# Optimization experiments

Hardware: AMD Instinct MI355X
Metric: run time of the kernel (lower is better)

## Reference

```python
import jax, jax.numpy as jnp
import numpy as np

N_OUT = 4096
N_IN = 4096
NNZ = 1600000
BATCH = 4096


def setup_inputs() -> dict:
    key = jax.random.key(0)
    k1, k2, k3, k4, k5 = jax.random.split(key, 5)
    inputs = jax.random.normal(k1, (N_IN, BATCH), dtype=jnp.float32)
    values = jax.random.normal(k2, (NNZ,), dtype=jnp.float32)
    biases = jax.random.normal(k3, (N_OUT, 1), dtype=jnp.float32)
    rows = jax.random.randint(k4, (NNZ,), 0, N_OUT, dtype=jnp.int32)
    cols = jax.random.randint(k5, (NNZ,), 0, N_IN, dtype=jnp.int32)
    return {"inputs": inputs, "values": values, "biases": biases,
            "rows": rows, "cols": cols}


def reference(inputs, values, biases, rows, cols):
    # torch.sparse.addmm(biases, W_sparse, inputs) with W COO [N_OUT, N_IN].
    # Scatter-add COO entries into a dense weight (duplicates summed, matching
    # coalesce semantics), then one dense GEMM -- avoids an [NNZ, BATCH]
    # gather intermediate while computing identical math.
    W = jnp.zeros((N_OUT, N_IN), dtype=values.dtype).at[rows, cols].add(values)
    out = W @ inputs + biases  # [N_OUT, BATCH], bias broadcast over columns
    return jax.nn.relu(out)    # activation epilogue
```

## Files before the change

### kernel.cpp

```cpp
#include <hip/hip_runtime.h>
#include <stdint.h>

#define N_OUT_  4096
#define N_IN_   4096
#define BATCH_  4096
#define NNZ_    1600000

typedef unsigned short ushort_t;
typedef float  f32x4  __attribute__((ext_vector_type(4)));
typedef short  short8 __attribute__((ext_vector_type(8)));
typedef __bf16 bf16x8 __attribute__((ext_vector_type(8)));

__device__ inline ushort_t f32_to_bf16(float f) {
  uint32_t u = __float_as_uint(f);
  uint32_t r = u + 0x7FFFu + ((u >> 16) & 1u);
  return (ushort_t)(r >> 16);
}
__device__ inline float bf16_to_f32(ushort_t h) {
  return __uint_as_float(((uint32_t)h) << 16);
}

__device__ inline void gload_lds16(const void* g, void* l) {
  __builtin_amdgcn_global_load_lds(
      (const __attribute__((address_space(1))) void*)g,
      (__attribute__((address_space(3))) void*)l,
      16, 0, 0);
}

__device__ inline f32x4 mfma_bf16(short8 a, short8 b, f32x4 c) {
  return __builtin_amdgcn_mfma_f32_16x16x32_bf16(
      __builtin_bit_cast(bf16x8, a), __builtin_bit_cast(bf16x8, b), c, 0, 0, 0);
}

#define BARRIER() asm volatile("s_barrier" ::: "memory")
template <int N> __device__ __forceinline__ void waitvm() {
  if constexpr (N == 8)      asm volatile("s_waitcnt vmcnt(8)" ::: "memory");
  else if constexpr (N == 6) asm volatile("s_waitcnt vmcnt(6)" ::: "memory");
  else if constexpr (N == 4) asm volatile("s_waitcnt vmcnt(4)" ::: "memory");
  else                       asm volatile("s_waitcnt vmcnt(0)" ::: "memory");
}

__global__ __launch_bounds__(256) void scatter_coo_cas(
    const float* __restrict__ vals, const int* __restrict__ rows,
    const int* __restrict__ cols, uint32_t* __restrict__ W32) {
  int i = blockIdx.x * 256 + threadIdx.x;
  if (i >= NNZ_) return;
  const size_t idx = (size_t)rows[i] * N_IN_ + cols[i];
  const float v = vals[i];
  uint32_t* p = &W32[idx >> 1];
  const bool hi = (idx & 1) != 0;
  uint32_t old = *p, assumed;
  do {
    assumed = old;
    ushort_t h = hi ? (ushort_t)(assumed >> 16) : (ushort_t)(assumed & 0xFFFFu);
    ushort_t nh = f32_to_bf16(bf16_to_f32(h) + v);
    uint32_t nw = hi ? ((assumed & 0x0000FFFFu) | ((uint32_t)nh << 16))
                     : ((assumed & 0xFFFF0000u) | (uint32_t)nh);
    old = atomicCAS(p, assumed, nw);
  } while (old != assumed);
}

__global__ __launch_bounds__(256) void transpose_bf16(
    const float* __restrict__ in, ushort_t* __restrict__ out) {
  __shared__ float tile[32][33];
  const int bx = blockIdx.x * 32, by = blockIdx.y * 32;
  const int tx = threadIdx.x, ty = threadIdx.y;
#pragma unroll
  for (int i = 0; i < 32; i += 8)
    tile[ty + i][tx] = in[(size_t)(by + ty + i) * BATCH_ + bx + tx];
  __syncthreads();
#pragma unroll
  for (int i = 0; i < 32; i += 8)
    out[(size_t)(bx + ty + i) * N_IN_ + by + tx] = f32_to_bf16(tile[tx][ty + i]);
}

#define BM 256
#define BN 256
#define BK 32
#define KTILES 128
#define TILE_BYTES 32768
#define B_OFF 16384

__global__ __launch_bounds__(512, 2) void gemm_bias_relu(
    const ushort_t* __restrict__ A,
    const ushort_t* __restrict__ Bt,
    const float* __restrict__ bias,
    float* __restrict__ C) {
  __shared__ __align__(16) char smem[4 * TILE_BYTES];

  const int tid  = threadIdx.x;
  const int wid  = tid >> 6;
  const int lane = tid & 63;

  const int bid = blockIdx.x;
  const int swz = (bid & 7) * 32 + (bid >> 3);
  const int brow = (swz >> 4) * BM;
  const int bcol = (swz & 15) * BN;

  const int wr = wid >> 2;
  const int wc = wid & 3;
  const int fr = lane & 15;
  const int k0slot = lane >> 4;

  int aoff[8], boff[4];
#pragma unroll
  for (int mi = 0; mi < 8; ++mi) {
    int off = (wr * 128 + mi * 16 + fr) * 64 + k0slot * 16;
    aoff[mi] = off ^ (((off >> 7) & 3) << 4);
  }
#pragma unroll
  for (int ni = 0; ni < 4; ++ni) {
    int off = (wc * 64 + ni * 16 + fr) * 64 + k0slot * 16;
    boff[ni] = off ^ (((off >> 7) & 3) << 4);
  }

  const bool isB = wid >= 4;
  const int sw = isB ? wid - 4 : wid;
  const int swzl = lane ^ ((lane >> 3) & 3);
  const int rowInChunk = swzl >> 2;
  const int kelem = (swzl & 3) * 8;
  const ushort_t* gsrc = isB ? Bt : A;
  const size_t laneRowBase =
      (size_t)((isB ? bcol : brow) + sw * 64 + rowInChunk) * N_IN_ + kelem;
  const int ldsOpBase = isB ? B_OFF : 0;

#define STAGE(p, i, t)                                                        \
  gload_lds16(gsrc + laneRowBase + (size_t)(2 * (p) + (i)) * 16 * N_IN_ +     \
                  (size_t)(t) * BK,                                           \
              smem + ((t) & 3) * TILE_BYTES + ldsOpBase +                     \
                  (4 * sw + 2 * (p) + (i)) * 1024)

  f32x4 acc[8][4] = {};
  short8 aE[4], bE[4], aO[4], bO[4], aH[4];

#pragma unroll
  for (int t = 0; t < 3; ++t) {
    STAGE(0, 0, t); STAGE(0, 1, t); STAGE(1, 0, t); STAGE(1, 1, t);
  }
  waitvm<8>();
  BARRIER();
#pragma unroll
  for (int j = 0; j < 4; ++j) {
    aE[j] = *(const short8*)(smem + aoff[j]);
    bE[j] = *(const short8*)(smem + B_OFF + boff[j]);
  }

#define TILE(t, AL, BB, ALn, BBn, S_ON, VM, RA_ON)                            \
  do {                                                                        \
    const char* buf  = &smem[((t) & 3) * TILE_BYTES];                         \
    const char* bufn = &smem[(((t) + 1) & 3) * TILE_BYTES];                   \
                                                                      \
    _Pragma("unroll") for (int j = 0; j < 4; ++j)                             \
        aH[j] = *(const short8*)(buf + aoff[j + 4]);                          \
    if (S_ON) { STAGE(0, 0, (t) + 3); STAGE(0, 1, (t) + 3); }                 \
    VM;                                                                       \
    BARRIER();                                                                \
    if (RA_ON) {                                                              \
      _Pragma("unroll") for (int j = 0; j < 4; ++j)                           \
          ALn[j] = *(const short8*)(bufn + aoff[j]);                          \
    }                                                                         \
    __builtin_amdgcn_s_setprio(1);                                            \
    _Pragma("unroll") for (int mi = 0; mi < 4; ++mi)                          \
        _Pragma("unroll") for (int ni = 0; ni < 4; ++ni)                      \
            acc[mi][ni] = mfma_bf16(AL[mi], BB[ni], acc[mi][ni]);             \
    __builtin_amdgcn_s_setprio(0);                                            \
    BARRIER();                                                                \
                                                                      \
    if (RA_ON) {                                                              \
      _Pragma("unroll") for (int j = 0; j < 4; ++j)                           \
          BBn[j] = *(const short8*)(bufn + B_OFF + boff[j]);                  \
    }                                                                         \
    if (S_ON) { STAGE(1, 0, (t) + 3); STAGE(1, 1, (t) + 3); }                 \
    BARRIER();                                                                \
    __builtin_amdgcn_s_setprio(1);                                            \
    _Pragma("unroll") for (int mi = 0; mi < 4; ++mi)                          \
        _Pragma("unroll") for (int ni = 0; ni < 4; ++ni)                      \
            acc[mi + 4][ni] = mfma_bf16(aH[mi], BB[ni], acc[mi + 4][ni]);     \
    __builtin_amdgcn_s_setprio(0);                                            \
    BARRIER();                                                                \
  } while (0)

  for (int t = 0; t < KTILES - 4; t += 2) {
    TILE(t,     aE, bE, aO, bO, 1, waitvm<6>(), 1);
    TILE(t + 1, aO, bO, aE, bE, 1, waitvm<6>(), 1);
  }
  TILE(KTILES - 4, aE, bE, aO, bO, 1, waitvm<6>(), 1);
  TILE(KTILES - 3, aO, bO, aE, bE, 0, waitvm<4>(), 1);
  TILE(KTILES - 2, aE, bE, aO, bO, 0, waitvm<0>(), 1);
  TILE(KTILES - 1, aO, bO, aE, bE, 0, (void)0,     0);

  const int r0 = brow + wr * 128 + k0slot * 4;
  const int c0 = bcol + wc * 64 + fr;
#pragma unroll
  for (int mi = 0; mi < 8; ++mi) {
#pragma unroll
    for (int r = 0; r < 4; ++r) {
      const int row = r0 + mi * 16 + r;
      const float b = bias[row];
#pragma unroll
      for (int ni = 0; ni < 4; ++ni) {
        float v = acc[mi][ni][r] + b;
        C[(size_t)row * BATCH_ + c0 + ni * 16] = v > 0.f ? v : 0.f;
      }
    }
  }
#undef TILE
#undef STAGE
}

extern "C" void kernel_launch(void* const* d_in, const int* in_sizes, int n_in,
                              void* d_out, int out_size, void* d_ws, size_t ws_size,
                              hipStream_t stream) {
  const float* inputs = (const float*)d_in[0];
  const float* values = (const float*)d_in[1];
  const float* biases = (const float*)d_in[2];
  const int*   rows   = (const int*)d_in[3];
  const int*   cols   = (const int*)d_in[4];
  float* out = (float*)d_out;

  const size_t W_BF16_BYTES = (size_t)N_OUT_ * N_IN_ * 2;
  if (ws_size < 2 * W_BF16_BYTES) return;
  char* ws = (char*)d_ws;
  ushort_t* Wb = (ushort_t*)ws;
  ushort_t* Bt = (ushort_t*)(ws + W_BF16_BYTES);

  hipMemsetAsync(Wb, 0, W_BF16_BYTES, stream);
  scatter_coo_cas<<<(NNZ_ + 255) / 256, 256, 0, stream>>>(values, rows, cols,
                                                          (uint32_t*)Wb);
  transpose_bf16<<<dim3(BATCH_ / 32, N_IN_ / 32), dim3(32, 8), 0, stream>>>(inputs, Bt);
  gemm_bias_relu<<<dim3(256), 512, 0, stream>>>(Wb, Bt, biases, out);
}
```

Before: 217.7 us.

## Restructure GEMM main loop into two-tile pairs with one barrier per tile

Replaces the ping-pong register-prefetch pipeline, which had split half-tile MFMA phases and three barriers per K tile, with a simpler scheme. Each K tile now issues all four global-to-LDS stage loads at once, reads the full A and B fragments from LDS, then runs all 32 MFMAs. Tiles are processed in pairs behind a single vmcnt wait and barrier, with one more barrier between the two tiles. This cuts barrier and wait overhead, but gives up the overlap of next-tile LDS reads with the current tile's MFMAs, so LDS latency may be exposed.

```diff
diff --git a/kernel.cpp b/kernel.cpp
--- a/kernel.cpp
+++ b/kernel.cpp
@@ -35,7 +35,6 @@
 #define BARRIER() asm volatile("s_barrier" ::: "memory")
 template <int N> __device__ __forceinline__ void waitvm() {
   if constexpr (N == 8)      asm volatile("s_waitcnt vmcnt(8)" ::: "memory");
-  else if constexpr (N == 6) asm volatile("s_waitcnt vmcnt(6)" ::: "memory");
   else if constexpr (N == 4) asm volatile("s_waitcnt vmcnt(4)" ::: "memory");
   else                       asm volatile("s_waitcnt vmcnt(0)" ::: "memory");
 }
@@ -124,70 +123,44 @@
       (size_t)((isB ? bcol : brow) + sw * 64 + rowInChunk) * N_IN_ + kelem;
   const int ldsOpBase = isB ? B_OFF : 0;
 
-#define STAGE(p, i, t)                                                        \
-  gload_lds16(gsrc + laneRowBase + (size_t)(2 * (p) + (i)) * 16 * N_IN_ +     \
-                  (size_t)(t) * BK,                                           \
+#define STAGE(c, t)                                                           \
+  gload_lds16(gsrc + laneRowBase + (size_t)(c) * 16 * N_IN_ + (size_t)(t) * BK,\
               smem + ((t) & 3) * TILE_BYTES + ldsOpBase +                     \
-                  (4 * sw + 2 * (p) + (i)) * 1024)
+                  (4 * sw + (c)) * 1024)
+#define STAGE4(t) do { STAGE(0,(t)); STAGE(1,(t)); STAGE(2,(t)); STAGE(3,(t)); } while (0)
 
   f32x4 acc[8][4] = {};
-  short8 aE[4], bE[4], aO[4], bO[4], aH[4];
-
-#pragma unroll
-  for (int t = 0; t < 3; ++t) {
-    STAGE(0, 0, t); STAGE(0, 1, t); STAGE(1, 0, t); STAGE(1, 1, t);
-  }
-  waitvm<8>();
-  BARRIER();
-#pragma unroll
-  for (int j = 0; j < 4; ++j) {
-    aE[j] = *(const short8*)(smem + aoff[j]);
-    bE[j] = *(const short8*)(smem + B_OFF + boff[j]);
-  }
-
-#define TILE(t, AL, BB, ALn, BBn, S_ON, VM, RA_ON)                            \
+  short8 af[8], bf[4];
+
+  STAGE4(0); STAGE4(1); STAGE4(2);
+
+#define HALF(t, S_ON, ST)                                                     \
   do {                                                                        \
-    const char* buf  = &smem[((t) & 3) * TILE_BYTES];                         \
-    const char* bufn = &smem[(((t) + 1) & 3) * TILE_BYTES];                   \
-                                                                      \
-    _Pragma("unroll") for (int j = 0; j < 4; ++j)                             \
-        aH[j] = *(const short8*)(buf + aoff[j + 4]);                          \
-    if (S_ON) { STAGE(0, 0, (t) + 3); STAGE(0, 1, (t) + 3); }                 \
+    const char* buf = &smem[((t) & 3) * TILE_BYTES];                          \
+    if (S_ON) STAGE4(ST);                                                     \
+    _Pragma("unroll") for (int ni = 0; ni < 4; ++ni)                          \
+        bf[ni] = *(const short8*)(buf + B_OFF + boff[ni]);                    \
+    _Pragma("unroll") for (int mi = 0; mi < 8; ++mi)                          \
+        af[mi] = *(const short8*)(buf + aoff[mi]);                            \
+    __builtin_amdgcn_s_setprio(1);                                            \
+    _Pragma("unroll") for (int mi = 0; mi < 8; ++mi)                          \
+        _Pragma("unroll") for (int ni = 0; ni < 4; ++ni)                      \
+            acc[mi][ni] = mfma_bf16(af[mi], bf[ni], acc[mi][ni]);             \
+    __builtin_amdgcn_s_setprio(0);                                            \
+  } while (0)
+
+#define PAIR(t, S1, S2, VM)                                                   \
+  do {                                                                        \
     VM;                                                                       \
     BARRIER();                                                                \
-    if (RA_ON) {                                                              \
-      _Pragma("unroll") for (int j = 0; j < 4; ++j)                           \
-          ALn[j] = *(const short8*)(bufn + aoff[j]);                          \
-    }                                                                         \
-    __builtin_amdgcn_s_setprio(1);                                            \
-    _Pragma("unroll") for (int mi = 0; mi < 4; ++mi)                          \
-        _Pragma("unroll") for (int ni = 0; ni < 4; ++ni)                      \
-            acc[mi][ni] = mfma_bf16(AL[mi], BB[ni], acc[mi][ni]);             \
-    __builtin_amdgcn_s_setprio(0);                                            \
+    HALF((t), S1, (t) + 3);                                                   \
     BARRIER();                                                                \
-                                                                      \
-    if (RA_ON) {                                                              \
-      _Pragma("unroll") for (int j = 0; j < 4; ++j)                           \
-          BBn[j] = *(const short8*)(bufn + B_OFF + boff[j]);                  \
-    }                                                                         \
-    if (S_ON) { STAGE(1, 0, (t) + 3); STAGE(1, 1, (t) + 3); }                 \
-    BARRIER();                                                                \
-    __builtin_amdgcn_s_setprio(1);                                            \
-    _Pragma("unroll") for (int mi = 0; mi < 4; ++mi)                          \
-        _Pragma("unroll") for (int ni = 0; ni < 4; ++ni)                      \
-            acc[mi + 4][ni] = mfma_bf16(aH[mi], BB[ni], acc[mi + 4][ni]);     \
-    __builtin_amdgcn_s_setprio(0);                                            \
-    BARRIER();                                                                \
+    HALF((t) + 1, S2, (t) + 4);                                               \
   } while (0)
 
-  for (int t = 0; t < KTILES - 4; t += 2) {
-    TILE(t,     aE, bE, aO, bO, 1, waitvm<6>(), 1);
-    TILE(t + 1, aO, bO, aE, bE, 1, waitvm<6>(), 1);
-  }
-  TILE(KTILES - 4, aE, bE, aO, bO, 1, waitvm<6>(), 1);
-  TILE(KTILES - 3, aO, bO, aE, bE, 0, waitvm<4>(), 1);
-  TILE(KTILES - 2, aE, bE, aO, bO, 0, waitvm<0>(), 1);
-  TILE(KTILES - 1, aO, bO, aE, bE, 0, (void)0,     0);
+  for (int t = 0; t < KTILES - 4; t += 2) PAIR(t, 1, 1, waitvm<4>());
+  PAIR(KTILES - 4, 1, 0, waitvm<4>());
+  PAIR(KTILES - 2, 0, 0, waitvm<0>());
 
   const int r0 = brow + wr * 128 + k0slot * 4;
   const int c0 = bcol + wc * 64 + fr;
@@ -204,7 +177,9 @@
       }
     }
   }
-#undef TILE
+#undef PAIR
+#undef HALF
+#undef STAGE4
 #undef STAGE
 }
 
```

Measured after the change: 210.6 us. 1.03x faster.

## Switch GEMM to 32x32x16 MFMA and fuse memset with input transpose

Applied to the files above, without the earlier changes.

The GEMM inner loop now uses 32x32x16 bf16 MFMA tiles in place of 16x16x32. This halves the number of MFMA instructions and changes the fragment offsets, the accumulator layout and the epilogue indexing. The tile schedule is reworked: two barriers are removed per k-tile, and the LDS reads for the next tile are interleaved between the two MFMA clusters. Separately, the workspace memset and the transpose/bf16 conversion are merged into one kernel launch, saving launch and serialization overhead at the risk of a subtly wrong fragment mapping.

```diff
diff --git a/kernel.cpp b/kernel.cpp
--- a/kernel.cpp
+++ b/kernel.cpp
@@ -7,7 +7,7 @@
 #define NNZ_    1600000
 
 typedef unsigned short ushort_t;
-typedef float  f32x4  __attribute__((ext_vector_type(4)));
+typedef float  f32x16 __attribute__((ext_vector_type(16)));
 typedef short  short8 __attribute__((ext_vector_type(8)));
 typedef __bf16 bf16x8 __attribute__((ext_vector_type(8)));
 
@@ -27,8 +27,8 @@
       16, 0, 0);
 }
 
-__device__ inline f32x4 mfma_bf16(short8 a, short8 b, f32x4 c) {
-  return __builtin_amdgcn_mfma_f32_16x16x32_bf16(
+__device__ inline f32x16 mfma32_bf16(short8 a, short8 b, f32x16 c) {
+  return __builtin_amdgcn_mfma_f32_32x32x16_bf16(
       __builtin_bit_cast(bf16x8, a), __builtin_bit_cast(bf16x8, b), c, 0, 0, 0);
 }
 
@@ -60,18 +60,29 @@
   } while (old != assumed);
 }
 
-__global__ __launch_bounds__(256) void transpose_bf16(
-    const float* __restrict__ in, ushort_t* __restrict__ out) {
-  __shared__ float tile[32][33];
-  const int bx = blockIdx.x * 32, by = blockIdx.y * 32;
-  const int tx = threadIdx.x, ty = threadIdx.y;
-#pragma unroll
-  for (int i = 0; i < 32; i += 8)
-    tile[ty + i][tx] = in[(size_t)(by + ty + i) * BATCH_ + bx + tx];
-  __syncthreads();
-#pragma unroll
-  for (int i = 0; i < 32; i += 8)
-    out[(size_t)(bx + ty + i) * N_IN_ + by + tx] = f32_to_bf16(tile[tx][ty + i]);
+#define TR_BLOCKS 16384
+#define MS_BLOCKS 2048
+__global__ __launch_bounds__(256) void prep_fused(
+    const float* __restrict__ in, ushort_t* __restrict__ out,
+    uint4* __restrict__ Wb4) {
+  const int b = blockIdx.x;
+  if (b < TR_BLOCKS) {
+    __shared__ float tile[32][33];
+    const int bx = (b & 127) * 32, by = (b >> 7) * 32;
+    const int tx = threadIdx.x & 31, ty = threadIdx.x >> 5;
+#pragma unroll
+    for (int i = 0; i < 32; i += 8)
+      tile[ty + i][tx] = in[(size_t)(by + ty + i) * BATCH_ + bx + tx];
+    __syncthreads();
+#pragma unroll
+    for (int i = 0; i < 32; i += 8)
+      out[(size_t)(bx + ty + i) * N_IN_ + by + tx] = f32_to_bf16(tile[tx][ty + i]);
+  } else {
+    const uint4 z = {0u, 0u, 0u, 0u};
+    const int idx = (b - TR_BLOCKS) * 256 + threadIdx.x;
+#pragma unroll
+    for (int j = 0; j < 4; ++j) Wb4[idx + j * (MS_BLOCKS * 256)] = z;
+  }
 }
 
 #define BM 256
@@ -99,20 +110,24 @@
 
   const int wr = wid >> 2;
   const int wc = wid & 3;
-  const int fr = lane & 15;
-  const int k0slot = lane >> 4;
+  const int ln31 = lane & 31;
+  const int hi5  = lane >> 5;
 
   int aoff[8], boff[4];
 #pragma unroll
-  for (int mi = 0; mi < 8; ++mi) {
-    int off = (wr * 128 + mi * 16 + fr) * 64 + k0slot * 16;
-    aoff[mi] = off ^ (((off >> 7) & 3) << 4);
-  }
-#pragma unroll
-  for (int ni = 0; ni < 4; ++ni) {
-    int off = (wc * 64 + ni * 16 + fr) * 64 + k0slot * 16;
-    boff[ni] = off ^ (((off >> 7) & 3) << 4);
-  }
+  for (int rb = 0; rb < 4; ++rb)
+#pragma unroll
+    for (int ks = 0; ks < 2; ++ks) {
+      int off = (wr * 128 + rb * 32 + ln31) * 64 + ks * 32 + hi5 * 16;
+      aoff[rb * 2 + ks] = off ^ (((off >> 7) & 3) << 4);
+    }
+#pragma unroll
+  for (int cb = 0; cb < 2; ++cb)
+#pragma unroll
+    for (int ks = 0; ks < 2; ++ks) {
+      int off = (wc * 64 + cb * 32 + ln31) * 64 + ks * 32 + hi5 * 16;
+      boff[cb * 2 + ks] = off ^ (((off >> 7) & 3) << 4);
+    }
 
   const bool isB = wid >= 4;
   const int sw = isB ? wid - 4 : wid;
@@ -124,19 +139,16 @@
       (size_t)((isB ? bcol : brow) + sw * 64 + rowInChunk) * N_IN_ + kelem;
   const int ldsOpBase = isB ? B_OFF : 0;
 
-#define STAGE(p, i, t)                                                        \
-  gload_lds16(gsrc + laneRowBase + (size_t)(2 * (p) + (i)) * 16 * N_IN_ +     \
-                  (size_t)(t) * BK,                                           \
+#define STAGE(c, t)                                                           \
+  gload_lds16(gsrc + laneRowBase + (size_t)(c) * 16 * N_IN_ + (size_t)(t) * BK,\
               smem + ((t) & 3) * TILE_BYTES + ldsOpBase +                     \
-                  (4 * sw + 2 * (p) + (i)) * 1024)
-
-  f32x4 acc[8][4] = {};
+                  (4 * sw + (c)) * 1024)
+
+  f32x16 acc[4][2] = {};
   short8 aE[4], bE[4], aO[4], bO[4], aH[4];
 
 #pragma unroll
-  for (int t = 0; t < 3; ++t) {
-    STAGE(0, 0, t); STAGE(0, 1, t); STAGE(1, 0, t); STAGE(1, 1, t);
-  }
+  for (int t = 0; t < 3; ++t) { STAGE(0, t); STAGE(1, t); STAGE(2, t); STAGE(3, t); }
   waitvm<8>();
   BARRIER();
 #pragma unroll
@@ -144,39 +156,37 @@
     aE[j] = *(const short8*)(smem + aoff[j]);
     bE[j] = *(const short8*)(smem + B_OFF + boff[j]);
   }
+
+#define CLUSTER(RB0, AF, BB)                                                  \
+  do {                                                                        \
+    __builtin_amdgcn_s_setprio(1);                                            \
+    _Pragma("unroll") for (int rb = 0; rb < 2; ++rb)                          \
+        _Pragma("unroll") for (int cb = 0; cb < 2; ++cb)                      \
+            _Pragma("unroll") for (int ks = 0; ks < 2; ++ks)                  \
+                acc[(RB0) + rb][cb] =                                         \
+                    mfma32_bf16(AF[rb * 2 + ks], BB[cb * 2 + ks],             \
+                                acc[(RB0) + rb][cb]);                         \
+    __builtin_amdgcn_s_setprio(0);                                            \
+  } while (0)
 
 #define TILE(t, AL, BB, ALn, BBn, S_ON, VM, RA_ON)                            \
   do {                                                                        \
     const char* buf  = &smem[((t) & 3) * TILE_BYTES];                         \
     const char* bufn = &smem[(((t) + 1) & 3) * TILE_BYTES];                   \
-                                                                      \
     _Pragma("unroll") for (int j = 0; j < 4; ++j)                             \
         aH[j] = *(const short8*)(buf + aoff[j + 4]);                          \
-    if (S_ON) { STAGE(0, 0, (t) + 3); STAGE(0, 1, (t) + 3); }                 \
+    if (S_ON) { STAGE(0, (t) + 3); STAGE(1, (t) + 3); }                       \
     VM;                                                                       \
     BARRIER();                                                                \
+    CLUSTER(0, AL, BB);                                                       \
     if (RA_ON) {                                                              \
       _Pragma("unroll") for (int j = 0; j < 4; ++j)                           \
           ALn[j] = *(const short8*)(bufn + aoff[j]);                          \
-    }                                                                         \
-    __builtin_amdgcn_s_setprio(1);                                            \
-    _Pragma("unroll") for (int mi = 0; mi < 4; ++mi)                          \
-        _Pragma("unroll") for (int ni = 0; ni < 4; ++ni)                      \
-            acc[mi][ni] = mfma_bf16(AL[mi], BB[ni], acc[mi][ni]);             \
-    __builtin_amdgcn_s_setprio(0);                                            \
-    BARRIER();                                                                \
-                                                                      \
-    if (RA_ON) {                                                              \
       _Pragma("unroll") for (int j = 0; j < 4; ++j)                           \
           BBn[j] = *(const short8*)(bufn + B_OFF + boff[j]);                  \
     }                                                                         \
-    if (S_ON) { STAGE(1, 0, (t) + 3); STAGE(1, 1, (t) + 3); }                 \
-    BARRIER();                                                                \
-    __builtin_amdgcn_s_setprio(1);                                            \
-    _Pragma("unroll") for (int mi = 0; mi < 4; ++mi)                          \
-        _Pragma("unroll") for (int ni = 0; ni < 4; ++ni)                      \
-            acc[mi + 4][ni] = mfma_bf16(aH[mi], BB[ni], acc[mi + 4][ni]);     \
-    __builtin_amdgcn_s_setprio(0);                                            \
+    if (S_ON) { STAGE(2, (t) + 3); STAGE(3, (t) + 3); }                       \
+    CLUSTER(2, aH, BB);                                                       \
     BARRIER();                                                                \
   } while (0)
 
@@ -189,22 +199,22 @@
   TILE(KTILES - 2, aE, bE, aO, bO, 0, waitvm<0>(), 1);
   TILE(KTILES - 1, aO, bO, aE, bE, 0, (void)0,     0);
 
-  const int r0 = brow + wr * 128 + k0slot * 4;
-  const int c0 = bcol + wc * 64 + fr;
-#pragma unroll
-  for (int mi = 0; mi < 8; ++mi) {
-#pragma unroll
-    for (int r = 0; r < 4; ++r) {
-      const int row = r0 + mi * 16 + r;
+#pragma unroll
+  for (int rb = 0; rb < 4; ++rb) {
+#pragma unroll
+    for (int reg = 0; reg < 16; ++reg) {
+      const int row = brow + wr * 128 + rb * 32 + (reg & 3) + 8 * (reg >> 2) + 4 * hi5;
       const float b = bias[row];
 #pragma unroll
-      for (int ni = 0; ni < 4; ++ni) {
-        float v = acc[mi][ni][r] + b;
-        C[(size_t)row * BATCH_ + c0 + ni * 16] = v > 0.f ? v : 0.f;
+      for (int cb = 0; cb < 2; ++cb) {
+        const int col = bcol + wc * 64 + cb * 32 + ln31;
+        float v = acc[rb][cb][reg] + b;
+        C[(size_t)row * BATCH_ + col] = v > 0.f ? v : 0.f;
       }
     }
   }
 #undef TILE
+#undef CLUSTER
 #undef STAGE
 }
 
@@ -224,9 +234,8 @@
   ushort_t* Wb = (ushort_t*)ws;
   ushort_t* Bt = (ushort_t*)(ws + W_BF16_BYTES);
 
-  hipMemsetAsync(Wb, 0, W_BF16_BYTES, stream);
+  prep_fused<<<TR_BLOCKS + MS_BLOCKS, 256, 0, stream>>>(inputs, Bt, (uint4*)Wb);
   scatter_coo_cas<<<(NNZ_ + 255) / 256, 256, 0, stream>>>(values, rows, cols,
                                                           (uint32_t*)Wb);
-  transpose_bf16<<<dim3(BATCH_ / 32, N_IN_ / 32), dim3(32, 8), 0, stream>>>(inputs, Bt);
   gemm_bias_relu<<<dim3(256), 512, 0, stream>>>(Wb, Bt, biases, out);
 }
```

Measured after the change: 214.8 us. No clear change (-1.3%).
